# Optimization experiments

Measured on AMD Instinct MI355X. Metric: run time of the kernel, lower is better.

Reference implementation:

```python
import jax, jax.numpy as jnp
import numpy as np

# Scalars from init_kwargs (qat_training=False inference path)
IN_ZP = 0
OUT_ZP = 0
IN_SCALE = 0.02
OUT_SCALE = 0.05
STRIDE = (1, 1)
PAD = (1, 1)      # (ph, pw); module pads (pw, pw, ph, ph) via F.pad
DIL = (1, 1)
GROUPS = 1
QMIN, QMAX = -128, 127  # get_quantized_range(8)


def setup_inputs() -> dict:
    key = jax.random.key(0)
    k1, k2, k3, k4 = jax.random.split(key, 4)
    x = jax.random.randint(k1, (32, 128, 56, 56), -128, 128, dtype=jnp.int32).astype(jnp.int8)
    weight = jax.random.randint(k2, (256, 128, 3, 3), -128, 128, dtype=jnp.int32).astype(jnp.int8)
    bias = jax.random.randint(k3, (256,), -1000, 1000, dtype=jnp.int32)
    weight_scale = jax.random.uniform(k4, (256,), minval=1e-3, maxval=1e-2, dtype=jnp.float32)
    return {"x": x, "weight": weight, "bias": bias, "weight_scale": weight_scale}


def reference(x, weight, bias, weight_scale):
    # Pad spatial dims with the input zero point (matches F.pad(..., value=input_zero_point))
    xp = jnp.pad(x.astype(jnp.int32),
                 ((0, 0), (0, 0), (PAD[0], PAD[0]), (PAD[1], PAD[1])),
                 constant_values=IN_ZP)
    # Exact int32-accumulate convolution (torch CPU path)
    acc = jax.lax.conv_general_dilated(
        xp, weight.astype(jnp.int32),
        window_strides=STRIDE, padding='VALID', rhs_dilation=DIL,
        dimension_numbers=('NCHW', 'OIHW', 'NCHW'),
        feature_group_count=GROUPS, preferred_element_type=jnp.int32)
    acc = acc + bias[None, :, None, None]
    # Per-output-channel requantization
    scale = (IN_SCALE * weight_scale / OUT_SCALE)[None, :, None, None]
    out = acc.astype(jnp.float32) * scale + OUT_ZP
    out = jnp.clip(jnp.round(out), QMIN, QMAX).astype(jnp.int8)
    return out
```

## Files before the change

kernel.cpp:

```cpp
#include <hip/hip_runtime.h>
#include <hip/hip_bf16.h>
#include <stdint.h>


#define NB   32
#define CIN  128
#define HO   56
#define WO   56
#define KOUT 256
#define HP   58
#define ROWB (HP * CIN)

typedef int v4i  __attribute__((ext_vector_type(4)));
typedef int v16i __attribute__((ext_vector_type(16)));

static __device__ __forceinline__ void gload_lds16(const int8_t* g, int8_t* l) {
  __builtin_amdgcn_global_load_lds(
      (const __attribute__((address_space(1))) void*)g,
      (__attribute__((address_space(3))) void*)l, 16, 0, 0);
}

__global__ __launch_bounds__(256) void pack_x_kernel(const int* __restrict__ x,
                                                     int8_t* __restrict__ xp) {
  __shared__ int t32[128][57];
  const int tid = threadIdx.x;
  const int r = blockIdx.x;
  const int n = blockIdx.y;
  const bool interior = (r >= 1) && (r <= HO);

  if (interior) {
    const int h = r - 1;
    const int* xrow = x + ((size_t)(n * CIN) * HO + h) * WO;
    #pragma unroll
    for (int it = 0; it < 7; ++it) {
      const int j = it * 256 + tid;
      const int c = j / 14;
      const int w4 = j - c * 14;
      const int4 v = *reinterpret_cast<const int4*>(xrow + c * 3136 + w4 * 4);
      t32[c][w4 * 4 + 0] = v.x;
      t32[c][w4 * 4 + 1] = v.y;
      t32[c][w4 * 4 + 2] = v.z;
      t32[c][w4 * 4 + 3] = v.w;
    }
  }
  __syncthreads();
  #pragma unroll
  for (int it = 0; it < 2; ++it) {
    const int i = it * 256 + tid;
    if (i < HP * 8) {
      const int w = i >> 3;
      const int q = i & 7;
      int4 vv; vv.x = 0; vv.y = 0; vv.z = 0; vv.w = 0;
      if (interior && w >= 1 && w <= WO) {
        int vals[4];
        #pragma unroll
        for (int ci = 0; ci < 4; ++ci) {
          const int c4 = q * 4 + ci;
          const int b0 = t32[c4 * 4 + 0][w - 1] & 0xff;
          const int b1 = t32[c4 * 4 + 1][w - 1] & 0xff;
          const int b2 = t32[c4 * 4 + 2][w - 1] & 0xff;
          const int b3 = t32[c4 * 4 + 3][w - 1];
          vals[ci] = b0 | (b1 << 8) | (b2 << 16) | (b3 << 24);
        }
        vv.x = vals[0]; vv.y = vals[1]; vv.z = vals[2]; vv.w = vals[3];
      }
      *reinterpret_cast<int4*>(xp + ((size_t)(n * HP + r) * HP + w) * CIN + q * 16) = vv;
    }
  }
}

__global__ __launch_bounds__(256) void pack_w_kernel(const int* __restrict__ wgt,
                                                     int8_t* __restrict__ wq) {
  const int wid = blockIdx.x * 256 + threadIdx.x;
  const int wi = wid & 3;
  const int ci = wid >> 2;
  const int kt = ci / 4608;
  const int r  = ci - kt * 4608;
  const int tap = r >> 9;
  const int r2  = r & 511;
  const int cc  = r2 >> 6;
  const int ch  = r2 & 63;
  const int k_global = kt * 64 + ch;
  const int cin0 = cc * 16 + wi * 4;
  const int base = (k_global * CIN + cin0) * 9 + tap;
  const int v0 = wgt[base];
  const int v1 = wgt[base + 9];
  const int v2 = wgt[base + 18];
  const int v3 = wgt[base + 27];
  reinterpret_cast<int*>(wq)[wid] =
      (v0 & 0xff) | ((v1 & 0xff) << 8) | ((v2 & 0xff) << 16) | (v3 << 24);
}

__global__ __launch_bounds__(448) void conv_kernel(const int8_t* __restrict__ xp,
                                                   const int8_t* __restrict__ wq,
                                                   const int* __restrict__ bias,
                                                   const float* __restrict__ wscale,
                                                   int* __restrict__ out) {
  __shared__ __align__(16) int8_t lw[9 * 8 * 64 * 16];
  __shared__ __align__(16) int8_t lx[9 * HP * 8 * 16];
  __shared__ int   bsh[64];
  __shared__ float ssh[64];

  const int tid = threadIdx.x;
  const int kt = blockIdx.x;
  const int h0 = blockIdx.y * 7;
  const int n_img = blockIdx.z;

  const int lane = tid & 63;
  const int wr = tid >> 6;
  const int p0 = lane & 31;
  const int half = lane >> 5;

  const int8_t* xg = xp + ((size_t)(n_img * HP) + h0) * ROWB;
  const int8_t* wqt = wq + (size_t)kt * 73728;

  #pragma unroll
  for (int it = 0; it < 11; ++it) {
    const int j = it * 448 + tid;
    if (j < 4608) gload_lds16(wqt + j * 16, lw + j * 16);
  }
  #pragma unroll
  for (int it = 0; it < 10; ++it) {
    const int i = it * 448 + tid;
    if (i < 9 * HP * 8) {
      const int pf = i >> 3;
      const int cc = (i & 7) ^ (pf & 7);
      gload_lds16(xg + pf * CIN + (cc << 4), lx + i * 16);
    }
  }
  if (tid < 64) {
    const int ch = kt * 64 + tid;
    bsh[tid] = bias[ch];
    ssh[tid] = (0.02f * wscale[ch]) / 0.05f;
  }
  __syncthreads();

  v16i acc[2][2];
  #pragma unroll
  for (int mt = 0; mt < 2; ++mt)
    #pragma unroll
    for (int nt = 0; nt < 2; ++nt)
      #pragma unroll
      for (int e = 0; e < 16; ++e) acc[mt][nt][e] = 0;

  #pragma unroll
  for (int tap = 0; tap < 9; ++tap) {
    const int kh = tap / 3, kw = tap % 3;
    const int8_t* lwt = lw + tap * 8192;
    const int pfb = (wr + kh) * HP + kw;
    #pragma unroll
    for (int ks = 0; ks < 4; ++ks) {
      const int cch = 2 * ks + half;
      const v4i a0 = *reinterpret_cast<const v4i*>(lwt + cch * 1024 + p0 * 16);
      const v4i a1 = *reinterpret_cast<const v4i*>(lwt + cch * 1024 + (32 + p0) * 16);
      #pragma unroll
      for (int nt = 0; nt < 2; ++nt) {
        const int pf = pfb + nt * 32 + p0;
        const v4i b = *reinterpret_cast<const v4i*>(
            lx + pf * CIN + ((cch ^ (pf & 7)) << 4));
        acc[0][nt] = __builtin_amdgcn_mfma_i32_32x32x32_i8(a0, b, acc[0][nt], 0, 0, 0);
        acc[1][nt] = __builtin_amdgcn_mfma_i32_32x32x32_i8(a1, b, acc[1][nt], 0, 0, 0);
      }
    }
  }

  const int h = h0 + wr;
  #pragma unroll
  for (int mt = 0; mt < 2; ++mt) {
    #pragma unroll
    for (int r = 0; r < 16; ++r) {
      const int cl = mt * 32 + (r & 3) + 8 * (r >> 2) + 4 * half;
      const int bi = bsh[cl];
      const float sc = ssh[cl];
      int* ob = out + (((size_t)(n_img * KOUT + kt * 64 + cl)) * HO + h) * WO;
      #pragma unroll
      for (int nt = 0; nt < 2; ++nt) {
        const int w = nt * 32 + p0;
        if (w < WO) {
          float v = (float)(acc[mt][nt][r] + bi) * sc;
          v = rintf(v);
          v = fminf(fmaxf(v, -128.0f), 127.0f);
          ob[w] = (int)v;
        }
      }
    }
  }
}

extern "C" void kernel_launch(void* const* d_in, const int* in_sizes, int n_in,
                              void* d_out, int out_size, void* d_ws, size_t ws_size,
                              hipStream_t stream) {
  const int* x = (const int*)d_in[0];
  const int* wgt = (const int*)d_in[1];
  const int* bias = (const int*)d_in[2];
  const float* wscale = (const float*)d_in[3];
  int* out = (int*)d_out;

  int8_t* xp = (int8_t*)d_ws;
  int8_t* wq = (int8_t*)d_ws + (size_t)NB * HP * ROWB;

  pack_x_kernel<<<dim3(HP, NB), 256, 0, stream>>>(x, xp);
  pack_w_kernel<<<288, 256, 0, stream>>>(wgt, wq);
  conv_kernel<<<dim3(4, 8, 32), 448, 0, stream>>>(xp, wq, bias, wscale, out);
}
```

Measured before the change: 186.5 us.

## Process four images per conv block, reusing staged weights and overlapping epilogue

Each conv block now handles four images instead of one. The 73 KB weight tile is loaded into LDS once per block and reused across all four images, cutting the weight traffic to a quarter. Two accumulator sets alternate so that the epilogue stores for one image are emitted after the next image's activations are staged. In exchange the grid shrinks from 1024 to 256 blocks, which may underfill the GPU's compute units, and the doubled accumulators raise register pressure. The pack_w bit masking is also rewritten with equivalent results.

```diff
diff --git a/kernel.cpp b/kernel.cpp
--- a/kernel.cpp
+++ b/kernel.cpp
@@ -88,7 +88,7 @@
   const int v2 = wgt[base + 18];
   const int v3 = wgt[base + 27];
   reinterpret_cast<int*>(wq)[wid] =
-      (v0 & 0xff) | ((v1 & 0xff) << 8) | ((v2 & 0xff) << 16) | (v3 << 24);
+      (v0 & 0xff) | ((v1 << 8) & 0xff00) | ((v2 << 16) & 0xff0000) | (v3 << 24);
 }
 
 __global__ __launch_bounds__(448) void conv_kernel(const int8_t* __restrict__ xp,
@@ -104,14 +104,13 @@
   const int tid = threadIdx.x;
   const int kt = blockIdx.x;
   const int h0 = blockIdx.y * 7;
-  const int n_img = blockIdx.z;
+  const int n0 = blockIdx.z * 4;
 
   const int lane = tid & 63;
   const int wr = tid >> 6;
   const int p0 = lane & 31;
   const int half = lane >> 5;
 
-  const int8_t* xg = xp + ((size_t)(n_img * HP) + h0) * ROWB;
   const int8_t* wqt = wq + (size_t)kt * 73728;
 
   #pragma unroll
@@ -119,72 +118,106 @@
     const int j = it * 448 + tid;
     if (j < 4608) gload_lds16(wqt + j * 16, lw + j * 16);
   }
-  #pragma unroll
-  for (int it = 0; it < 10; ++it) {
-    const int i = it * 448 + tid;
-    if (i < 9 * HP * 8) {
-      const int pf = i >> 3;
-      const int cc = (i & 7) ^ (pf & 7);
-      gload_lds16(xg + pf * CIN + (cc << 4), lx + i * 16);
-    }
-  }
   if (tid < 64) {
     const int ch = kt * 64 + tid;
     bsh[tid] = bias[ch];
     ssh[tid] = (0.02f * wscale[ch]) / 0.05f;
   }
-  __syncthreads();
-
-  v16i acc[2][2];
-  #pragma unroll
-  for (int mt = 0; mt < 2; ++mt)
-    #pragma unroll
-    for (int nt = 0; nt < 2; ++nt)
-      #pragma unroll
-      for (int e = 0; e < 16; ++e) acc[mt][nt][e] = 0;
-
-  #pragma unroll
-  for (int tap = 0; tap < 9; ++tap) {
-    const int kh = tap / 3, kw = tap % 3;
-    const int8_t* lwt = lw + tap * 8192;
-    const int pfb = (wr + kh) * HP + kw;
-    #pragma unroll
-    for (int ks = 0; ks < 4; ++ks) {
-      const int cch = 2 * ks + half;
-      const v4i a0 = *reinterpret_cast<const v4i*>(lwt + cch * 1024 + p0 * 16);
-      const v4i a1 = *reinterpret_cast<const v4i*>(lwt + cch * 1024 + (32 + p0) * 16);
-      #pragma unroll
-      for (int nt = 0; nt < 2; ++nt) {
-        const int pf = pfb + nt * 32 + p0;
-        const v4i b = *reinterpret_cast<const v4i*>(
-            lx + pf * CIN + ((cch ^ (pf & 7)) << 4));
-        acc[0][nt] = __builtin_amdgcn_mfma_i32_32x32x32_i8(a0, b, acc[0][nt], 0, 0, 0);
-        acc[1][nt] = __builtin_amdgcn_mfma_i32_32x32x32_i8(a1, b, acc[1][nt], 0, 0, 0);
-      }
-    }
-  }
-
-  const int h = h0 + wr;
-  #pragma unroll
-  for (int mt = 0; mt < 2; ++mt) {
-    #pragma unroll
-    for (int r = 0; r < 16; ++r) {
-      const int cl = mt * 32 + (r & 3) + 8 * (r >> 2) + 4 * half;
-      const int bi = bsh[cl];
-      const float sc = ssh[cl];
-      int* ob = out + (((size_t)(n_img * KOUT + kt * 64 + cl)) * HO + h) * WO;
-      #pragma unroll
-      for (int nt = 0; nt < 2; ++nt) {
-        const int w = nt * 32 + p0;
-        if (w < WO) {
-          float v = (float)(acc[mt][nt][r] + bi) * sc;
-          v = rintf(v);
-          v = fminf(fmaxf(v, -128.0f), 127.0f);
-          ob[w] = (int)v;
-        }
-      }
-    }
-  }
+
+#define STAGE_LX(i)                                                           \
+  {                                                                           \
+    const int8_t* xg = xp + ((size_t)((n0 + (i)) * HP) + h0) * ROWB;          \
+    _Pragma("unroll")                                                         \
+    for (int it = 0; it < 10; ++it) {                                         \
+      const int j = it * 448 + tid;                                           \
+      if (j < 9 * HP * 8) {                                                   \
+        const int pf = j >> 3;                                                \
+        const int cc = (j & 7) ^ (pf & 7);                                    \
+        gload_lds16(xg + pf * CIN + (cc << 4), lx + j * 16);                  \
+      }                                                                       \
+    }                                                                         \
+  }
+
+#define KLOOP(acc)                                                            \
+  {                                                                           \
+    _Pragma("unroll")                                                         \
+    for (int mt = 0; mt < 2; ++mt)                                            \
+      _Pragma("unroll")                                                       \
+      for (int nt = 0; nt < 2; ++nt)                                          \
+        _Pragma("unroll")                                                     \
+        for (int e = 0; e < 16; ++e) acc[mt][nt][e] = 0;                      \
+    _Pragma("unroll")                                                         \
+    for (int tap = 0; tap < 9; ++tap) {                                       \
+      const int kh = tap / 3, kw = tap % 3;                                   \
+      const int8_t* lwt = lw + tap * 8192;               \
+      const int pfb = (wr + kh) * HP + kw;                                    \
+      _Pragma("unroll")                                                       \
+      for (int ks = 0; ks < 4; ++ks) {                                        \
+        const int cch = 2 * ks + half;                                        \
+        const v4i a0 = *reinterpret_cast<const v4i*>(lwt + cch * 1024 + p0 * 16); \
+        const v4i a1 = *reinterpret_cast<const v4i*>(lwt + cch * 1024 + (32 + p0) * 16); \
+        _Pragma("unroll")                                                     \
+        for (int nt = 0; nt < 2; ++nt) {                                      \
+          const int pf = pfb + nt * 32 + p0;                                  \
+          const v4i b = *reinterpret_cast<const v4i*>(                        \
+              lx + pf * CIN + ((cch ^ (pf & 7)) << 4));                       \
+          acc[0][nt] = __builtin_amdgcn_mfma_i32_32x32x32_i8(a0, b, acc[0][nt], 0, 0, 0); \
+          acc[1][nt] = __builtin_amdgcn_mfma_i32_32x32x32_i8(a1, b, acc[1][nt], 0, 0, 0); \
+        }                                                                     \
+      }                                                                       \
+    }                                                                         \
+  }
+
+#define EPILOGUE(acc, i)                                                      \
+  {                                                                           \
+    const int h = h0 + wr;                                                    \
+    _Pragma("unroll")                                                         \
+    for (int mt = 0; mt < 2; ++mt) {                                          \
+      _Pragma("unroll")                                                       \
+      for (int r = 0; r < 16; ++r) {                                          \
+        const int cl = mt * 32 + (r & 3) + 8 * (r >> 2) + 4 * half;           \
+        const int bi = bsh[cl];                                               \
+        const float sc = ssh[cl];                                             \
+        int* ob = out + (((size_t)((n0 + (i)) * KOUT + kt * 64 + cl)) * HO + h) * WO; \
+        _Pragma("unroll")                                                     \
+        for (int nt = 0; nt < 2; ++nt) {                                      \
+          const int w = nt * 32 + p0;                                         \
+          if (w < WO) {                                                       \
+            float v = (float)(acc[mt][nt][r] + bi) * sc;                      \
+            v = rintf(v);                               \
+            v = fminf(fmaxf(v, -128.0f), 127.0f);                             \
+            ob[w] = (int)v;                                                   \
+          }                                                                   \
+        }                                                                     \
+      }                                                                       \
+    }                                                                         \
+  }
+
+  v16i accA[2][2], accB[2][2];
+
+  STAGE_LX(0);
+  __syncthreads();
+  KLOOP(accA);
+  __syncthreads();
+  STAGE_LX(1);
+  __syncthreads();
+  EPILOGUE(accA, 0);
+  KLOOP(accB);
+  __syncthreads();
+  STAGE_LX(2);
+  __syncthreads();
+  EPILOGUE(accB, 1);
+  KLOOP(accA);
+  __syncthreads();
+  STAGE_LX(3);
+  __syncthreads();
+  EPILOGUE(accA, 2);
+  KLOOP(accB);
+  EPILOGUE(accB, 3);
+
+#undef STAGE_LX
+#undef KLOOP
+#undef EPILOGUE
 }
 
 extern "C" void kernel_launch(void* const* d_in, const int* in_sizes, int n_in,
@@ -201,5 +234,5 @@
 
   pack_x_kernel<<<dim3(HP, NB), 256, 0, stream>>>(x, xp);
   pack_w_kernel<<<288, 256, 0, stream>>>(wgt, wq);
-  conv_kernel<<<dim3(4, 8, 32), 448, 0, stream>>>(xp, wq, bias, wscale, out);
-}
+  conv_kernel<<<dim3(4, 8, 8), 448, 0, stream>>>(xp, wq, bias, wscale, out);
+}
```

Measured after the change: 185.5 us. About the same (-0.5%).
